# Optimization experiments

Hardware: AMD Instinct MI355X
Metric: run time of the kernel (lower is better)

Reference implementation:

```python
import jax, jax.numpy as jnp
import numpy as np

MAX_SCALE = 10  # matches init_kwargs max_scale


def setup_inputs() -> dict:
    key = jax.random.key(0)
    # [B, H, W, D, C] as consumed by keras MaxPooling3D (channels_last)
    x = jax.random.normal(key, (8, 224, 224, 8, 8), dtype=jnp.float32)
    return {"x": x}


def reference(x):
    # For each scale s in 1..MAX_SCALE: max-pool over (H, W) with an s x s
    # window, stride 1, VALID padding (pool dim 3 has window 1), then sum the
    # pooled map over the two pooled spatial axes -> [B, D, C].
    boxes_at_scale = []
    for scale in range(1, MAX_SCALE + 1):
        pooled = jax.lax.reduce_window(
            x,
            -jnp.inf,
            jax.lax.max,
            window_dimensions=(1, scale, scale, 1, 1),
            window_strides=(1, 1, 1, 1, 1),
            padding="VALID",
        )  # [B, H-s+1, W-s+1, D, C]
        boxes_at_scale.append(jnp.sum(pooled, axis=(1, 2)))  # [B, D, C]
    stacked = jnp.stack(boxes_at_scale, axis=-1)  # [B, D, C, MAX_SCALE]
    return jax.nn.relu(stacked) + 1.0
```

## Files before the change

kernel.cpp:

```cpp
#include <hip/hip_runtime.h>

#define BB 8
#define HH 224
#define WW 224
#define DCH 64
#define NS 10
#define SEG 55
#define NSEG 5
#define STRIP 28
#define NHS 8
#define NCG 8
#define NBLK (BB * NCG * NSEG * NHS)

__global__ void zero_kernel(float* out, int n) {
    int i = blockIdx.x * blockDim.x + threadIdx.x;
    if (i < n) out[i] = 0.0f;
}

__global__ void finalize_kernel(float* out, int n) {
    int i = blockIdx.x * blockDim.x + threadIdx.x;
    if (i < n) out[i] = fmaxf(out[i], 0.0f) + 1.0f;
}

__device__ __forceinline__ float dpp_shl1(float v) {
    return __int_as_float(__builtin_amdgcn_mov_dpp(__float_as_int(v), 0x130, 0xF, 0xF, true));
}

template<int PHASE>
__device__ __forceinline__ void row_body(int h, int row0, const float (&m)[NS],
                                         float (&cp)[2], float (&prev)[NS - 1][2],
                                         float (&acc)[NS][2]) {
    if (PHASE != 2) {
        acc[0][0] = fmaf(cp[0], m[0], acc[0][0]);
        acc[0][1] = fmaf(cp[1], m[0], acc[0][1]);
    }
#pragma unroll
    for (int lv = 0; lv < NS - 1; ++lv) {
        float vm0 = fmaxf(prev[lv][0], cp[0]);
        float vm1 = fmaxf(prev[lv][1], cp[1]);
        prev[lv][0] = cp[0];
        prev[lv][1] = cp[1];
        cp[0] = fmaxf(vm0, dpp_shl1(vm0));
        cp[1] = fmaxf(vm1, dpp_shl1(vm1));
        bool on = true;
        if (PHASE == 0) on = (h - lv - 1) >= row0;
        if (PHASE == 2) on = (h - lv - 1) < row0 + STRIP;
        if (on) {
            acc[lv + 1][0] = fmaf(cp[0], m[lv + 1], acc[lv + 1][0]);
            acc[lv + 1][1] = fmaf(cp[1], m[lv + 1], acc[lv + 1][1]);
        }
    }
}

__global__ __launch_bounds__(256, 4) void pool_kernel(const float* __restrict__ x,
                                                      float* __restrict__ out) {
    const int phys = blockIdx.x;
    const int logical = (phys & 7) * (NBLK / 8) + (phys >> 3);
    const int b = logical / (NCG * NSEG * NHS);
    const int r = logical % (NCG * NSEG * NHS);
    const int cg = r & 7;
    const int ws = (r >> 3) % NSEG;
    const int hs = (r >> 3) / NSEG;

    const int wv   = threadIdx.x >> 6;
    const int lane = threadIdx.x & 63;
    const int ch   = cg * 8 + wv * 2;
    const int col  = ws * SEG + lane;
    const int row0 = hs * STRIP;
    const int rend = min(row0 + STRIP + NS - 1, HH);

    float m[NS];
#pragma unroll
    for (int s = 1; s <= NS; ++s)
        m[s - 1] = (lane < SEG && col <= WW - s) ? 1.0f : 0.0f;

    float prev[NS - 1][2], acc[NS][2], cp[2], nv[2];
#pragma unroll
    for (int lv = 0; lv < NS - 1; ++lv) { prev[lv][0] = 0.0f; prev[lv][1] = 0.0f; }
#pragma unroll
    for (int s = 0; s < NS; ++s) { acc[s][0] = 0.0f; acc[s][1] = 0.0f; }
    nv[0] = 0.0f; nv[1] = 0.0f;

    const bool colok = (col < WW);
    const float* px = x + (((size_t)(b * HH + row0) * WW + col) * DCH + ch);
    const ptrdiff_t rstride = (ptrdiff_t)WW * DCH;

    if (colok) { float2 t = *(const float2*)px; nv[0] = t.x; nv[1] = t.y; }

#define ROW_STEP(P)                                                          \
    {                                                                        \
        cp[0] = nv[0]; cp[1] = nv[1];                                        \
        if (h + 1 < rend) {   \
            px += rstride;                                                   \
            if (colok) { float2 t = *(const float2*)px; nv[0] = t.x; nv[1] = t.y; } \
        }                                                                    \
        row_body<P>(h, row0, m, cp, prev, acc);                              \
    }

    int h = row0;
    const int warm_end = row0 + NS - 1;
    for (; h < warm_end; ++h) ROW_STEP(0)
    const int steady_end = min(row0 + STRIP, rend);
    for (; h < steady_end; ++h) ROW_STEP(1)
    for (; h < rend; ++h) ROW_STEP(2)
#undef ROW_STEP

#pragma unroll
    for (int s = 0; s < NS; ++s) {
#pragma unroll
        for (int c = 0; c < 2; ++c) {
            float v = acc[s][c];
#pragma unroll
            for (int off = 32; off > 0; off >>= 1) v += __shfl_xor(v, off);
            if (lane == 0) atomicAdd(&out[((size_t)b * DCH + ch + c) * NS + s], v);
        }
    }
}

extern "C" void kernel_launch(void* const* d_in, const int* in_sizes, int n_in,
                              void* d_out, int out_size, void* d_ws, size_t ws_size,
                              hipStream_t stream) {
    const float* x = (const float*)d_in[0];
    float* out = (float*)d_out;
    const int nblk = (out_size + 255) / 256;
    zero_kernel<<<nblk, 256, 0, stream>>>(out, out_size);
    pool_kernel<<<NBLK, 256, 0, stream>>>(x, out);
    finalize_kernel<<<nblk, 256, 0, stream>>>(out, out_size);
}
```

Before: 206.5 us.

## Stage row loads through double-buffered LDS for coalesced global reads

Each row tile is now loaded cooperatively: four threads share one column and read its 8 contiguous channels, instead of each wave reading 2 channels per column at a 256-byte stride. The tile is transposed into a padded LDS double buffer and each wave reads its channel pair back. Global loads are prefetched one row ahead. The aim is to cut redundant cache-line traffic and improve load efficiency, at the cost of a __syncthreads and extra LDS traffic on every row.

```diff
diff --git a/kernel.cpp b/kernel.cpp
--- a/kernel.cpp
+++ b/kernel.cpp
@@ -11,6 +11,8 @@
 #define NHS 8
 #define NCG 8
 #define NBLK (BB * NCG * NSEG * NHS)
+#define PS 72
+#define LDSBUF (8 * PS)
 
 __global__ void zero_kernel(float* out, int n) {
     int i = blockIdx.x * blockDim.x + threadIdx.x;
@@ -54,6 +56,8 @@
 
 __global__ __launch_bounds__(256, 4) void pool_kernel(const float* __restrict__ x,
                                                       float* __restrict__ out) {
+    __shared__ float lds[2 * LDSBUF];
+
     const int phys = blockIdx.x;
     const int logical = (phys & 7) * (NBLK / 8) + (phys >> 3);
     const int b = logical / (NCG * NSEG * NHS);
@@ -74,27 +78,36 @@
     for (int s = 1; s <= NS; ++s)
         m[s - 1] = (lane < SEG && col <= WW - s) ? 1.0f : 0.0f;
 
-    float prev[NS - 1][2], acc[NS][2], cp[2], nv[2];
+    float prev[NS - 1][2], acc[NS][2], cp[2];
 #pragma unroll
     for (int lv = 0; lv < NS - 1; ++lv) { prev[lv][0] = 0.0f; prev[lv][1] = 0.0f; }
 #pragma unroll
     for (int s = 0; s < NS; ++s) { acc[s][0] = 0.0f; acc[s][1] = 0.0f; }
-    nv[0] = 0.0f; nv[1] = 0.0f;
 
-    const bool colok = (col < WW);
-    const float* px = x + (((size_t)(b * HH + row0) * WW + col) * DCH + ch);
+    const int scol = threadIdx.x >> 2;
+    const int q    = threadIdx.x & 3;
+    const int gcol = min(ws * SEG + scol, WW - 1);
+    const float* sp = x + (((size_t)(b * HH + row0) * WW + gcol) * DCH + cg * 8 + q * 2);
     const ptrdiff_t rstride = (ptrdiff_t)WW * DCH;
 
-    if (colok) { float2 t = *(const float2*)px; nv[0] = t.x; nv[1] = t.y; }
+    const int wbase = (2 * q) * PS + scol;
+    const int rbase = (2 * wv) * PS + lane;
 
-#define ROW_STEP(P)                                                          \
-    {                                                                        \
-        cp[0] = nv[0]; cp[1] = nv[1];                                        \
-        if (h + 1 < rend) {   \
-            px += rstride;                                                   \
-            if (colok) { float2 t = *(const float2*)px; nv[0] = t.x; nv[1] = t.y; } \
-        }                                                                    \
-        row_body<P>(h, row0, m, cp, prev, acc);                              \
+    { float2 t0 = *(const float2*)sp;
+      lds[wbase] = t0.x; lds[wbase + PS] = t0.y; }
+    sp += rstride;
+    float2 g = *(const float2*)sp;
+    int sb = 0;
+
+#define ROW_STEP(P)                                                           \
+    {                                                                         \
+        __syncthreads();                                                      \
+        const int so = sb ^ LDSBUF;                                           \
+        lds[so + wbase] = g.x; lds[so + wbase + PS] = g.y;       \
+        if (h + 2 < rend) { sp += rstride; g = *(const float2*)sp; }          \
+        cp[0] = lds[sb + rbase]; cp[1] = lds[sb + rbase + PS];     \
+        row_body<P>(h, row0, m, cp, prev, acc);                               \
+        sb = so;                                                              \
     }
 
     int h = row0;
```

New measurement: 192.4 us. -6.9%, faster.
